# Performance work log

Hardware: AMD Instinct MI355X
Metric: run time of the kernel (lower is better)

Reference implementation:

```python
import jax, jax.numpy as jnp
import numpy as np

N = 50000      # nodes
F_IN = 128     # node_features
T = 12         # periods
E = 800000     # edges (avg degree 16)
MID = 32       # mid_channels (fixed in __init__)
NEG_SLOPE = 0.01
EPS = 1e-12


def setup_inputs() -> dict:
    key = jax.random.key(0)
    ks = jax.random.split(key, 9)
    s_in = 1.0 / np.sqrt(F_IN)
    s_mid = 1.0 / np.sqrt(MID)
    return {
        "x": jax.random.normal(ks[0], (1, N, F_IN, T), jnp.float32),
        "edge_index": jax.random.randint(ks[1], (2, E), 0, N, jnp.int64),
        "edge_weight": jax.random.uniform(ks[2], (E,), jnp.float32),
        # SAGEConv params: lin_l (with bias) applied to aggregated neighbors, lin_r (no bias) to root
        "W_l": jax.random.uniform(ks[3], (MID, F_IN), jnp.float32, -s_in, s_in),
        "b_l": jax.random.uniform(ks[4], (MID,), jnp.float32, -s_in, s_in),
        "W_r": jax.random.uniform(ks[5], (MID, F_IN), jnp.float32, -s_in, s_in),
        "attention": jax.random.uniform(ks[6], (T,), jnp.float32),
        "lin_W": jax.random.uniform(ks[7], (1, MID), jnp.float32, -s_mid, s_mid),
        "lin_b": jax.random.uniform(ks[8], (1,), jnp.float32, -s_mid, s_mid),
    }


def reference(x, edge_index, edge_weight, W_l, b_l, W_r, attention, lin_W, lin_b):
    src, dst = edge_index[0], edge_index[1]
    # in-degree for mean aggregation (shared across periods)
    deg = jax.ops.segment_sum(jnp.ones((E,), x.dtype), dst, num_segments=N)
    inv_deg = 1.0 / jnp.clip(deg, 1.0)  # [N]

    def sage(xt):  # xt: [N, F_IN] -> [N, MID], SAGEConv(mean, normalize=True)
        agg = jax.ops.segment_sum(xt[src], dst, num_segments=N) * inv_deg[:, None]
        out = agg @ W_l.T + b_l + xt @ W_r.T
        norm = jnp.linalg.norm(out, axis=-1, keepdims=True)
        return out / jnp.maximum(norm, EPS)

    gk = jax.random.key(42)
    k1, k2 = jax.random.split(gk)
    # F.gumbel_softmax over the periods-attention vector (tau=1, soft)
    probs = jax.nn.softmax(attention + jax.random.gumbel(k1, (T,), x.dtype))

    h = jnp.zeros((N, MID), x.dtype)
    for t in range(T):  # small fixed unroll over periods
        h = h + probs[t] * sage(x[0, :, :, t])

    h = jnp.where(h > 0, h, NEG_SLOPE * h)        # leaky_relu
    h = h @ lin_W.T + lin_b                        # [N, 1]
    g2 = jax.random.gumbel(k2, h.shape, h.dtype)
    return jax.nn.softmax(h + g2, axis=0)          # gumbel_softmax over nodes
```

## Files before the change

### kernel.cpp

```cpp
#include <hip/hip_runtime.h>
#include <hip/hip_fp16.h>
#include <stdint.h>

#define N_NODES 50000
#define F_INF   128
#define T_P     12
#define N_EDGES 800000
#define MIDC    32
#define SCHUNK  782

typedef __attribute__((ext_vector_type(8))) short bf16x8;
typedef __attribute__((ext_vector_type(4))) float f32x4;

__device__ __forceinline__ uint32_t rotl32(uint32_t v, int r) {
  return (v << r) | (v >> (32 - r));
}

__device__ __forceinline__ void threefry(uint32_t k0, uint32_t k1,
                                         uint32_t x0, uint32_t x1,
                                         uint32_t& o0, uint32_t& o1) {
  uint32_t k2 = k0 ^ k1 ^ 0x1BD11BDAu;
  x0 += k0; x1 += k1;
#define TFR(r) { x0 += x1; x1 = rotl32(x1, r); x1 ^= x0; }
  TFR(13) TFR(15) TFR(26) TFR(6)
  x0 += k1; x1 += k2 + 1u;
  TFR(17) TFR(29) TFR(16) TFR(24)
  x0 += k2; x1 += k0 + 2u;
  TFR(13) TFR(15) TFR(26) TFR(6)
  x0 += k0; x1 += k1 + 3u;
  TFR(17) TFR(29) TFR(16) TFR(24)
  x0 += k1; x1 += k2 + 4u;
  TFR(13) TFR(15) TFR(26) TFR(6)
  x0 += k2; x1 += k0 + 5u;
#undef TFR
  o0 = x0; o1 = x1;
}

__device__ __forceinline__ float gumbel_from_bits(uint32_t bits) {
  const float TINY = 1.17549435082228751e-38f;
  float f = __uint_as_float((bits >> 9) | 0x3F800000u) - 1.0f;
  float u = fmaxf(TINY, f * (1.0f - TINY) + TINY);
  return -logf(-logf(u));
}

__device__ __forceinline__ uint32_t f2bf(float f) {
  uint32_t u = __float_as_uint(f);
  return (u + 0x7FFFu + ((u >> 16) & 1u)) >> 16;
}
__device__ __forceinline__ float bf2f(uint16_t v) {
  return __uint_as_float(((uint32_t)v) << 16);
}

__device__ __forceinline__ uint32_t f2e5m2(float v) {
  float ax = fabsf(v);
  uint32_t s = (__float_as_uint(v) >> 31) << 7;
  if (ax < 6.103515625e-5f) return s;
  ax = fminf(ax, 57344.0f);
  uint32_t u = __float_as_uint(ax);
  u += 0xFFFFFu + ((u >> 21) & 1u);
  uint32_t m = (u >> 21) & 3u;
  uint32_t E = (u >> 23) - 127u + 15u;
  return s | (E << 2) | m;
}

union HU { uint32_t u; __half2 h; };
__device__ __forceinline__ void acc_e5m2(uint32_t u, __half2& lo, __half2& hi) {
  HU a, b;
  a.u = (u << 8) & 0xff00ff00u;
  b.u = u & 0xff00ff00u;
  lo = __hadd2(lo, a.h);
  hi = __hadd2(hi, b.h);
}

__global__ void k_init(const float* __restrict__ att, const float* __restrict__ Wl,
                       const float* __restrict__ Wr,
                       float* __restrict__ header, uint16_t* __restrict__ wtb,
                       int* __restrict__ cnt, int* __restrict__ cursor,
                       float* __restrict__ psum) {
  int bid = blockIdx.x;
  if (bid == 0) {
    if (threadIdx.x == 0) {
      uint32_t a0, a1, b0, b1;
      threefry(0u, 42u, 0u, 0u, a0, a1);
      threefry(0u, 42u, 0u, 1u, b0, b1);
      float v[12], m = -3.4e38f;
      for (int t = 0; t < 12; ++t) {
        uint32_t o0, o1;
        threefry(a0, a1, 0u, (uint32_t)t, o0, o1);
        v[t] = att[t] + gumbel_from_bits(o0 ^ o1);
        m = fmaxf(m, v[t]);
      }
      float s = 0.f;
      for (int t = 0; t < 12; ++t) { v[t] = expf(v[t] - m); s += v[t]; }
      for (int t = 0; t < 12; ++t) header[t] = v[t] / s;
      uint32_t* hu = (uint32_t*)header;
      hu[16] = b0; hu[17] = b1;
    }
  } else if (bid <= 32) {
    int i = (bid - 1) * 256 + threadIdx.x;
    int cm = i >> 7, f = i & 127;
    float val = (cm < 32) ? Wl[cm * 128 + f] : Wr[(cm - 32) * 128 + f];
    wtb[i] = (uint16_t)f2bf(val);
  } else {
    int i = (bid - 33) * 256 + threadIdx.x;
    if (i < N_NODES) cnt[i] = 0;
    else if (i < 2 * N_NODES) cursor[i - N_NODES] = 0;
    else if (i < 2 * N_NODES + 64) psum[i - 2 * N_NODES] = 0.f;
  }
}

__global__ void k_scan1(const int* __restrict__ cnt, int* __restrict__ bsum) {
  __shared__ int sb[256];
  int b = blockIdx.x, tid = threadIdx.x;
  int start = b * SCHUNK, end = min(start + SCHUNK, N_NODES);
  int s = 0;
  for (int i = start + tid; i < end; i += 256) s += cnt[i];
  sb[tid] = s;
  __syncthreads();
  for (int o = 128; o > 0; o >>= 1) {
    if (tid < o) sb[tid] += sb[tid + o];
    __syncthreads();
  }
  if (tid == 0) bsum[b] = sb[0];
}

__global__ void k_scan2(const int* __restrict__ cnt, const int* __restrict__ bsum,
                        int* __restrict__ rowptr) {
  __shared__ int bs[64];
  __shared__ int sc[256];
  int b = blockIdx.x, tid = threadIdx.x;
  if (tid < 64) bs[tid] = bsum[tid];
  __syncthreads();
  int base = 0;
  for (int k = 0; k < b; ++k) base += bs[k];
  int bstart = b * SCHUNK, bend = min(bstart + SCHUNK, N_NODES);
  int istart = bstart + tid * 4;
  int iend = min(istart + 4, bend);
  int c[4]; int s = 0;
#pragma unroll
  for (int k = 0; k < 4; ++k) {
    int i = istart + k;
    c[k] = (i < bend) ? cnt[i] : 0;
    s += c[k];
  }
  sc[tid] = s;
  __syncthreads();
  for (int off = 1; off < 256; off <<= 1) {
    int v = (tid >= off) ? sc[tid - off] : 0;
    __syncthreads();
    sc[tid] += v;
    __syncthreads();
  }
  int run = base + sc[tid] - s;
#pragma unroll
  for (int k = 0; k < 4; ++k) {
    int i = istart + k;
    if (i < bend) { rowptr[i] = run; run += c[k]; }
  }
  if (iend == N_NODES) rowptr[N_NODES] = run;
}

__global__ void k_scatter(const int* __restrict__ src, const int* __restrict__ dst,
                          const int* __restrict__ rowptr, int* __restrict__ cursor,
                          int* __restrict__ col) {
  int e = blockIdx.x * blockDim.x + threadIdx.x;
  if (e < N_EDGES) {
    int d = dst[e];
    int pos = rowptr[d] + atomicAdd(&cursor[d], 1);
    col[pos] = src[e];
  }
}

__launch_bounds__(256)
__global__ void k_project(const float* __restrict__ x, const uint16_t* __restrict__ wtb,
                          const float* __restrict__ bl,
                          uint8_t* __restrict__ Y, uint16_t* __restrict__ OUTI,
                          const int* __restrict__ dst, int* __restrict__ cnt) {
  __shared__ uint32_t smem4[16384];
  char* sm = (char*)smem4;
  int tid = threadIdx.x;
  int node_base = blockIdx.x * 16;

  atomicAdd(&cnt[dst[blockIdx.x * 256 + tid]], 1);

  const uint32_t* wtb32 = (const uint32_t*)wtb;
#pragma unroll
  for (int i0 = 0; i0 < 16; ++i0) {
    int i = i0 * 256 + tid;
    uint32_t v = wtb32[i];
    int cm = i >> 6, c = i & 63;
    *(uint32_t*)(sm + 49152 + cm * 256 + ((c * 4) ^ ((cm & 7) << 4))) = v;
  }

#pragma unroll 4
  for (int i = 0; i < 12; ++i) {
    int p = i * 256 + tid;
    int node = p / 192;
    int rem  = p - node * 192;
    int fpair = rem / 3;
    int tg = rem - fpair * 3;
    const float* xb = x + (uint32_t)(node_base + node) * 1536u + fpair * 24 + tg * 4;
    float4 q0 = *(const float4*)xb;
    float4 q1 = *(const float4*)(xb + 12);
    int mb = node * 12 + tg * 4;
    const float* q0f = (const float*)&q0;
    const float* q1f = (const float*)&q1;
#pragma unroll
    for (int j = 0; j < 4; ++j) {
      int m = mb + j;
      uint32_t wv = f2bf(q0f[j]) | (f2bf(q1f[j]) << 16);
      *(uint32_t*)(sm + m * 256 + ((fpair * 4) ^ ((m & 7) << 4))) = wv;
    }
  }
  __syncthreads();

  int w = tid >> 6, l = tid & 63;
  int li = l & 15, kg = l >> 4;
  f32x4 acc[3][4];
#pragma unroll
  for (int mt = 0; mt < 3; ++mt)
#pragma unroll
    for (int nt = 0; nt < 4; ++nt)
      acc[mt][nt] = (f32x4){0.f, 0.f, 0.f, 0.f};

  const char* A = sm;
  const char* B = sm + 49152;
  __builtin_amdgcn_s_setprio(1);
#pragma unroll
  for (int ks = 0; ks < 4; ++ks) {
    int kb = ks * 64 + kg * 16;
    bf16x8 bf0, bf1, bf2, bf3;
    {
      int r0 = li,      s0 = kb ^ ((r0 & 7) << 4);
      int r1 = 16 + li, s1 = kb ^ ((r1 & 7) << 4);
      int r2 = 32 + li, s2 = kb ^ ((r2 & 7) << 4);
      int r3 = 48 + li, s3 = kb ^ ((r3 & 7) << 4);
      bf0 = *(const bf16x8*)(B + r0 * 256 + s0);
      bf1 = *(const bf16x8*)(B + r1 * 256 + s1);
      bf2 = *(const bf16x8*)(B + r2 * 256 + s2);
      bf3 = *(const bf16x8*)(B + r3 * 256 + s3);
    }
#pragma unroll
    for (int mt = 0; mt < 3; ++mt) {
      int row = w * 48 + mt * 16 + li;
      bf16x8 af = *(const bf16x8*)(A + row * 256 + (kb ^ ((row & 7) << 4)));
      acc[mt][0] = __builtin_amdgcn_mfma_f32_16x16x32_bf16(af, bf0, acc[mt][0], 0, 0, 0);
      acc[mt][1] = __builtin_amdgcn_mfma_f32_16x16x32_bf16(af, bf1, acc[mt][1], 0, 0, 0);
      acc[mt][2] = __builtin_amdgcn_mfma_f32_16x16x32_bf16(af, bf2, acc[mt][2], 0, 0, 0);
      acc[mt][3] = __builtin_amdgcn_mfma_f32_16x16x32_bf16(af, bf3, acc[mt][3], 0, 0, 0);
    }
  }
  __builtin_amdgcn_s_setprio(0);

  float bv0 = bl[li], bv1 = bl[16 + li];
#pragma unroll
  for (int mt = 0; mt < 3; ++mt) {
    int rbase = w * 48 + mt * 16 + kg * 4;
#pragma unroll
    for (int r = 0; r < 4; ++r) {
      int m = rbase + r;
      int node = m / 12;
      int t = m - node * 12;
      uint32_t rowoff = (uint32_t)(node_base + node) * 384u + t * 32;
      Y[rowoff + li]      = (uint8_t)f2e5m2(acc[mt][0][r]);
      Y[rowoff + 16 + li] = (uint8_t)f2e5m2(acc[mt][1][r]);
      OUTI[rowoff + li]      = (uint16_t)f2bf(acc[mt][2][r] + bv0);
      OUTI[rowoff + 16 + li] = (uint16_t)f2bf(acc[mt][3][r] + bv1);
    }
  }
}

__launch_bounds__(384)
__global__ void k_gather(const uint8_t* __restrict__ Y, const uint16_t* __restrict__ OUTI,
                         const int* __restrict__ rowptr, const int* __restrict__ col,
                         const float* __restrict__ header,
                         const float* __restrict__ linW, const float* __restrict__ linb,
                         float* __restrict__ out, float* __restrict__ psum) {
  __shared__ float hb[4][12][33];
  __shared__ float esum;
  int tid = threadIdx.x;
  int ln = tid / 96;
  int tc = tid - ln * 96;
  int n = blockIdx.x * 4 + ln;
  int t = tc >> 3, cq = tc & 7;
  if (tid == 0) esum = 0.f;

  int beg = rowptr[n], end = rowptr[n + 1];
  const uint32_t* Yp = reinterpret_cast<const uint32_t*>(Y);
  uint32_t utc = (uint32_t)tc;
  __half2 zl; { HU z; z.u = 0; zl = z.h; }
  __half2 alo = zl, ahi = zl, blo = zl, bhi = zl;
  int j = beg;
  for (; j < end && (j & 3); ++j)
    acc_e5m2(Yp[(uint32_t)col[j] * 96u + utc], alo, ahi);
  for (; j + 7 < end; j += 8) {
    int4 c0 = *reinterpret_cast<const int4*>(&col[j]);
    int4 c1 = *reinterpret_cast<const int4*>(&col[j + 4]);
    uint32_t u0 = Yp[(uint32_t)c0.x * 96u + utc];
    uint32_t u1 = Yp[(uint32_t)c0.y * 96u + utc];
    uint32_t u2 = Yp[(uint32_t)c0.z * 96u + utc];
    uint32_t u3 = Yp[(uint32_t)c0.w * 96u + utc];
    uint32_t u4 = Yp[(uint32_t)c1.x * 96u + utc];
    uint32_t u5 = Yp[(uint32_t)c1.y * 96u + utc];
    uint32_t u6 = Yp[(uint32_t)c1.z * 96u + utc];
    uint32_t u7 = Yp[(uint32_t)c1.w * 96u + utc];
    acc_e5m2(u0, alo, ahi); acc_e5m2(u1, blo, bhi);
    acc_e5m2(u2, alo, ahi); acc_e5m2(u3, blo, bhi);
    acc_e5m2(u4, alo, ahi); acc_e5m2(u5, blo, bhi);
    acc_e5m2(u6, alo, ahi); acc_e5m2(u7, blo, bhi);
  }
  for (; j + 3 < end; j += 4) {
    int4 c0 = *reinterpret_cast<const int4*>(&col[j]);
    uint32_t u0 = Yp[(uint32_t)c0.x * 96u + utc];
    uint32_t u1 = Yp[(uint32_t)c0.y * 96u + utc];
    uint32_t u2 = Yp[(uint32_t)c0.z * 96u + utc];
    uint32_t u3 = Yp[(uint32_t)c0.w * 96u + utc];
    acc_e5m2(u0, alo, ahi); acc_e5m2(u1, blo, bhi);
    acc_e5m2(u2, alo, ahi); acc_e5m2(u3, blo, bhi);
  }
  for (; j < end; ++j)
    acc_e5m2(Yp[(uint32_t)col[j] * 96u + utc], alo, ahi);
  alo = __hadd2(alo, blo); ahi = __hadd2(ahi, bhi);
  float a0 = __low2float(alo),  a2 = __high2float(alo);
  float a1 = __low2float(ahi),  a3 = __high2float(ahi);

  float invd = 1.0f / fmaxf((float)(end - beg), 1.0f);
  ushort4 ov = *reinterpret_cast<const ushort4*>(OUTI + (uint32_t)n * 384u + tc * 4);
  float v0 = bf2f(ov.x) + a0 * invd;
  float v1 = bf2f(ov.y) + a1 * invd;
  float v2 = bf2f(ov.z) + a2 * invd;
  float v3 = bf2f(ov.w) + a3 * invd;
  float sq = v0 * v0 + v1 * v1 + v2 * v2 + v3 * v3;
  sq += __shfl_xor(sq, 1);
  sq += __shfl_xor(sq, 2);
  sq += __shfl_xor(sq, 4);
  float rn = header[t] / fmaxf(sqrtf(sq), 1e-12f);
  float* hrow = &hb[ln][t][cq * 4];
  hrow[0] = v0 * rn; hrow[1] = v1 * rn; hrow[2] = v2 * rn; hrow[3] = v3 * rn;
  __syncthreads();
  if (tid < 128) {
    int ln2 = tid >> 5, c = tid & 31;
    float h = 0.f;
#pragma unroll
    for (int tt = 0; tt < 12; ++tt) h += hb[ln2][tt][c];
    h = (h > 0.f) ? h : 0.01f * h;
    float hv = h * linW[c];
#pragma unroll
    for (int m = 16; m >= 1; m >>= 1) hv += __shfl_xor(hv, m);
    if (c == 0) {
      int n2 = blockIdx.x * 4 + ln2;
      const uint32_t* hu = (const uint32_t*)header;
      uint32_t o0, o1;
      threefry(hu[16], hu[17], 0u, (uint32_t)n2, o0, o1);
      float ex = expf(hv + linb[0] + gumbel_from_bits(o0 ^ o1));
      out[n2] = ex;
      atomicAdd(&esum, ex);
    }
  }
  __syncthreads();
  if (tid == 0) atomicAdd(&psum[blockIdx.x & 63], esum);
}

__global__ void k_scale(float* __restrict__ out, const float* __restrict__ psum) {
  float S = 0.f;
#pragma unroll
  for (int k = 0; k < 64; ++k) S += psum[k];
  int i = blockIdx.x * blockDim.x + threadIdx.x;
  if (i < N_NODES) out[i] = out[i] / S;
}

extern "C" void kernel_launch(void* const* d_in, const int* in_sizes, int n_in,
                              void* d_out, int out_size, void* d_ws, size_t ws_size,
                              hipStream_t stream) {
  (void)in_sizes; (void)n_in; (void)out_size; (void)ws_size;
  const float* x    = (const float*)d_in[0];
  const int*   ei   = (const int*)d_in[1];
  const float* Wl   = (const float*)d_in[3];
  const float* bl   = (const float*)d_in[4];
  const float* Wr   = (const float*)d_in[5];
  const float* att  = (const float*)d_in[6];
  const float* linW = (const float*)d_in[7];
  const float* linb = (const float*)d_in[8];
  float* out = (float*)d_out;

  const int* esrc = ei;
  const int* edst = ei + N_EDGES;

  char* base = (char*)d_ws;
  size_t o = 0;
  auto take = [&](size_t b) { size_t r = o; o += (b + 255) & ~(size_t)255; return r; };
  float* header = (float*)(base + take(256));
  int*   cnt    = (int*)(base + take((size_t)N_NODES * 4));
  int*   cursor = (int*)(base + take((size_t)N_NODES * 4));
  int*   rowptr = (int*)(base + take((size_t)(N_NODES + 1) * 4));
  int*   col    = (int*)(base + take((size_t)N_EDGES * 4));
  int*   bsum   = (int*)(base + take(64 * 4));
  float* psum   = (float*)(base + take(64 * 4));
  uint16_t* wtb = (uint16_t*)(base + take(64 * 128 * 2));
  uint8_t*  Y   = (uint8_t*)(base + take((size_t)N_NODES * 384));
  uint16_t* OUTI= (uint16_t*)(base + take((size_t)N_NODES * 384 * 2));

  k_init<<<424, 256, 0, stream>>>(att, Wl, Wr, header, wtb, cnt, cursor, psum);
  k_project<<<N_NODES / 16, 256, 0, stream>>>(x, wtb, bl, Y, OUTI, edst, cnt);
  k_scan1<<<64, 256, 0, stream>>>(cnt, bsum);
  k_scan2<<<64, 256, 0, stream>>>(cnt, bsum, rowptr);
  k_scatter<<<(N_EDGES + 255) / 256, 256, 0, stream>>>(esrc, edst, rowptr, cursor, col);
  k_gather<<<N_NODES / 4, 384, 0, stream>>>(Y, OUTI, rowptr, col, header, linW, linb, out, psum);
  k_scale<<<(N_NODES + 255) / 256, 256, 0, stream>>>(out, psum);
}
```

Baseline: 241.7 us.

## Quantize projected neighbor features to FP4 e2m1 and widen gather per thread

Projected neighbor features, which the gather step reads randomly, are now stored as 4-bit e2m1 values instead of 8-bit e5m2. This halves the Y buffer and the bytes fetched per edge. The gather kernel decodes them with a byte-permute lookup into half2 accumulators and now handles 8 nodes per block, with each thread covering 8 channels. The projection epilogue uses a transposed MFMA operand order so that stores can be packed. The cursor reset moves from init into scan2. FP4 quantization of aggregated features is very coarse and risks accuracy failures against the reference.

```diff
diff --git a/kernel.cpp b/kernel.cpp
--- a/kernel.cpp
+++ b/kernel.cpp
@@ -51,32 +51,37 @@
   return __uint_as_float(((uint32_t)v) << 16);
 }
 
-__device__ __forceinline__ uint32_t f2e5m2(float v) {
+__device__ __forceinline__ uint32_t f2e2m1(float v) {
   float ax = fabsf(v);
-  uint32_t s = (__float_as_uint(v) >> 31) << 7;
-  if (ax < 6.103515625e-5f) return s;
-  ax = fminf(ax, 57344.0f);
-  uint32_t u = __float_as_uint(ax);
-  u += 0xFFFFFu + ((u >> 21) & 1u);
-  uint32_t m = (u >> 21) & 3u;
-  uint32_t E = (u >> 23) - 127u + 15u;
-  return s | (E << 2) | m;
+  uint32_t s = (__float_as_uint(v) >> 31) << 3;
+  if (ax < 0.75f) return s | (ax <= 0.25f ? 0u : 1u);
+  uint32_t u = __float_as_uint(fminf(fmaxf(ax, 1.0f), 6.0f));
+  u += 0x1FFFFFu + ((u >> 22) & 1u);
+  uint32_t m = (u >> 22) & 1u;
+  uint32_t E = (u >> 23) - 127u;
+  return s | (((E + 1u) << 1) | m);
 }
 
 union HU { uint32_t u; __half2 h; };
-__device__ __forceinline__ void acc_e5m2(uint32_t u, __half2& lo, __half2& hi) {
+__device__ __forceinline__ void acc_fp4(uint32_t u, __half2& e0, __half2& e1,
+                                        __half2& o0, __half2& o1) {
+  uint32_t ue = u & 0x0F0F0F0Fu;
+  uint32_t uo = (u >> 4) & 0x0F0F0F0Fu;
+  uint32_t pe = __builtin_amdgcn_perm(0x46444240u, 0x3E3C3800u, ue & 0x07070707u)
+              | ((ue & 0x08080808u) << 4);
+  uint32_t po = __builtin_amdgcn_perm(0x46444240u, 0x3E3C3800u, uo & 0x07070707u)
+              | ((uo & 0x08080808u) << 4);
   HU a, b;
-  a.u = (u << 8) & 0xff00ff00u;
-  b.u = u & 0xff00ff00u;
-  lo = __hadd2(lo, a.h);
-  hi = __hadd2(hi, b.h);
+  a.u = (pe << 8) & 0xff00ff00u; e0 = __hadd2(e0, a.h);
+  b.u = pe & 0xff00ff00u;        e1 = __hadd2(e1, b.h);
+  a.u = (po << 8) & 0xff00ff00u; o0 = __hadd2(o0, a.h);
+  b.u = po & 0xff00ff00u;        o1 = __hadd2(o1, b.h);
 }
 
 __global__ void k_init(const float* __restrict__ att, const float* __restrict__ Wl,
                        const float* __restrict__ Wr,
                        float* __restrict__ header, uint16_t* __restrict__ wtb,
-                       int* __restrict__ cnt, int* __restrict__ cursor,
-                       float* __restrict__ psum) {
+                       int* __restrict__ cnt, float* __restrict__ psum) {
   int bid = blockIdx.x;
   if (bid == 0) {
     if (threadIdx.x == 0) {
@@ -104,8 +109,7 @@
   } else {
     int i = (bid - 33) * 256 + threadIdx.x;
     if (i < N_NODES) cnt[i] = 0;
-    else if (i < 2 * N_NODES) cursor[i - N_NODES] = 0;
-    else if (i < 2 * N_NODES + 64) psum[i - 2 * N_NODES] = 0.f;
+    else if (i < N_NODES + 64) psum[i - N_NODES] = 0.f;
   }
 }
 
@@ -125,7 +129,7 @@
 }
 
 __global__ void k_scan2(const int* __restrict__ cnt, const int* __restrict__ bsum,
-                        int* __restrict__ rowptr) {
+                        int* __restrict__ rowptr, int* __restrict__ cursor) {
   __shared__ int bs[64];
   __shared__ int sc[256];
   int b = blockIdx.x, tid = threadIdx.x;
@@ -155,7 +159,7 @@
 #pragma unroll
   for (int k = 0; k < 4; ++k) {
     int i = istart + k;
-    if (i < bend) { rowptr[i] = run; run += c[k]; }
+    if (i < bend) { rowptr[i] = run; cursor[i] = 0; run += c[k]; }
   }
   if (iend == N_NODES) rowptr[N_NODES] = run;
 }
@@ -218,10 +222,10 @@
   int li = l & 15, kg = l >> 4;
   f32x4 acc[3][4];
 #pragma unroll
-  for (int mt = 0; mt < 3; ++mt)
-#pragma unroll
-    for (int nt = 0; nt < 4; ++nt)
-      acc[mt][nt] = (f32x4){0.f, 0.f, 0.f, 0.f};
+  for (int jt = 0; jt < 3; ++jt)
+#pragma unroll
+    for (int it = 0; it < 4; ++it)
+      acc[jt][it] = (f32x4){0.f, 0.f, 0.f, 0.f};
 
   const char* A = sm;
   const char* B = sm + 49152;
@@ -229,44 +233,52 @@
 #pragma unroll
   for (int ks = 0; ks < 4; ++ks) {
     int kb = ks * 64 + kg * 16;
-    bf16x8 bf0, bf1, bf2, bf3;
+    bf16x8 wf0, wf1, wf2, wf3;
     {
       int r0 = li,      s0 = kb ^ ((r0 & 7) << 4);
       int r1 = 16 + li, s1 = kb ^ ((r1 & 7) << 4);
       int r2 = 32 + li, s2 = kb ^ ((r2 & 7) << 4);
       int r3 = 48 + li, s3 = kb ^ ((r3 & 7) << 4);
-      bf0 = *(const bf16x8*)(B + r0 * 256 + s0);
-      bf1 = *(const bf16x8*)(B + r1 * 256 + s1);
-      bf2 = *(const bf16x8*)(B + r2 * 256 + s2);
-      bf3 = *(const bf16x8*)(B + r3 * 256 + s3);
-    }
-#pragma unroll
-    for (int mt = 0; mt < 3; ++mt) {
-      int row = w * 48 + mt * 16 + li;
-      bf16x8 af = *(const bf16x8*)(A + row * 256 + (kb ^ ((row & 7) << 4)));
-      acc[mt][0] = __builtin_amdgcn_mfma_f32_16x16x32_bf16(af, bf0, acc[mt][0], 0, 0, 0);
-      acc[mt][1] = __builtin_amdgcn_mfma_f32_16x16x32_bf16(af, bf1, acc[mt][1], 0, 0, 0);
-      acc[mt][2] = __builtin_amdgcn_mfma_f32_16x16x32_bf16(af, bf2, acc[mt][2], 0, 0, 0);
-      acc[mt][3] = __builtin_amdgcn_mfma_f32_16x16x32_bf16(af, bf3, acc[mt][3], 0, 0, 0);
+      wf0 = *(const bf16x8*)(B + r0 * 256 + s0);
+      wf1 = *(const bf16x8*)(B + r1 * 256 + s1);
+      wf2 = *(const bf16x8*)(B + r2 * 256 + s2);
+      wf3 = *(const bf16x8*)(B + r3 * 256 + s3);
+    }
+#pragma unroll
+    for (int jt = 0; jt < 3; ++jt) {
+      int row = w * 48 + jt * 16 + li;
+      bf16x8 xf = *(const bf16x8*)(A + row * 256 + (kb ^ ((row & 7) << 4)));
+      acc[jt][0] = __builtin_amdgcn_mfma_f32_16x16x32_bf16(wf0, xf, acc[jt][0], 0, 0, 0);
+      acc[jt][1] = __builtin_amdgcn_mfma_f32_16x16x32_bf16(wf1, xf, acc[jt][1], 0, 0, 0);
+      acc[jt][2] = __builtin_amdgcn_mfma_f32_16x16x32_bf16(wf2, xf, acc[jt][2], 0, 0, 0);
+      acc[jt][3] = __builtin_amdgcn_mfma_f32_16x16x32_bf16(wf3, xf, acc[jt][3], 0, 0, 0);
     }
   }
   __builtin_amdgcn_s_setprio(0);
 
-  float bv0 = bl[li], bv1 = bl[16 + li];
-#pragma unroll
-  for (int mt = 0; mt < 3; ++mt) {
-    int rbase = w * 48 + mt * 16 + kg * 4;
-#pragma unroll
-    for (int r = 0; r < 4; ++r) {
-      int m = rbase + r;
-      int node = m / 12;
-      int t = m - node * 12;
-      uint32_t rowoff = (uint32_t)(node_base + node) * 384u + t * 32;
-      Y[rowoff + li]      = (uint8_t)f2e5m2(acc[mt][0][r]);
-      Y[rowoff + 16 + li] = (uint8_t)f2e5m2(acc[mt][1][r]);
-      OUTI[rowoff + li]      = (uint16_t)f2bf(acc[mt][2][r] + bv0);
-      OUTI[rowoff + 16 + li] = (uint16_t)f2bf(acc[mt][3][r] + bv1);
-    }
+  float4 bla = *(const float4*)&bl[kg * 4];
+  float4 blb = *(const float4*)&bl[16 + kg * 4];
+#pragma unroll
+  for (int jt = 0; jt < 3; ++jt) {
+    int m = (w * 3 + jt) * 16 + li;
+    int node = m / 12;
+    int t = m - node * 12;
+    uint32_t rbY = (uint32_t)(node_base + node) * 192u + t * 16;
+#pragma unroll
+    for (int it = 0; it < 2; ++it) {
+      uint32_t p = 0;
+#pragma unroll
+      for (int r = 0; r < 4; ++r) p |= f2e2m1(acc[jt][it][r]) << (4 * r);
+      *(uint16_t*)(Y + rbY + it * 8 + kg * 2) = (uint16_t)p;
+    }
+    uint32_t rbO = (uint32_t)(node_base + node) * 384u + t * 32;
+    uint2 pk;
+    pk.x = f2bf(acc[jt][2][0] + bla.x) | (f2bf(acc[jt][2][1] + bla.y) << 16);
+    pk.y = f2bf(acc[jt][2][2] + bla.z) | (f2bf(acc[jt][2][3] + bla.w) << 16);
+    *(uint2*)(OUTI + rbO + kg * 4) = pk;
+    pk.x = f2bf(acc[jt][3][0] + blb.x) | (f2bf(acc[jt][3][1] + blb.y) << 16);
+    pk.y = f2bf(acc[jt][3][2] + blb.z) | (f2bf(acc[jt][3][3] + blb.w) << 16);
+    *(uint2*)(OUTI + rbO + 16 + kg * 4) = pk;
   }
 }
 
@@ -276,69 +288,77 @@
                          const float* __restrict__ header,
                          const float* __restrict__ linW, const float* __restrict__ linb,
                          float* __restrict__ out, float* __restrict__ psum) {
-  __shared__ float hb[4][12][33];
+  __shared__ float hb[8][12][33];
   __shared__ float esum;
   int tid = threadIdx.x;
-  int ln = tid / 96;
-  int tc = tid - ln * 96;
-  int n = blockIdx.x * 4 + ln;
-  int t = tc >> 3, cq = tc & 7;
+  int ln = tid / 48;
+  int tc = tid - ln * 48;
+  int n = blockIdx.x * 8 + ln;
+  int t = tc >> 2, cq = tc & 3;
   if (tid == 0) esum = 0.f;
 
   int beg = rowptr[n], end = rowptr[n + 1];
   const uint32_t* Yp = reinterpret_cast<const uint32_t*>(Y);
   uint32_t utc = (uint32_t)tc;
   __half2 zl; { HU z; z.u = 0; zl = z.h; }
-  __half2 alo = zl, ahi = zl, blo = zl, bhi = zl;
+  __half2 ae0 = zl, ae1 = zl, ao0 = zl, ao1 = zl;
+  __half2 be0 = zl, be1 = zl, bo0 = zl, bo1 = zl;
   int j = beg;
   for (; j < end && (j & 3); ++j)
-    acc_e5m2(Yp[(uint32_t)col[j] * 96u + utc], alo, ahi);
+    acc_fp4(Yp[(uint32_t)col[j] * 48u + utc], ae0, ae1, ao0, ao1);
   for (; j + 7 < end; j += 8) {
     int4 c0 = *reinterpret_cast<const int4*>(&col[j]);
     int4 c1 = *reinterpret_cast<const int4*>(&col[j + 4]);
-    uint32_t u0 = Yp[(uint32_t)c0.x * 96u + utc];
-    uint32_t u1 = Yp[(uint32_t)c0.y * 96u + utc];
-    uint32_t u2 = Yp[(uint32_t)c0.z * 96u + utc];
-    uint32_t u3 = Yp[(uint32_t)c0.w * 96u + utc];
-    uint32_t u4 = Yp[(uint32_t)c1.x * 96u + utc];
-    uint32_t u5 = Yp[(uint32_t)c1.y * 96u + utc];
-    uint32_t u6 = Yp[(uint32_t)c1.z * 96u + utc];
-    uint32_t u7 = Yp[(uint32_t)c1.w * 96u + utc];
-    acc_e5m2(u0, alo, ahi); acc_e5m2(u1, blo, bhi);
-    acc_e5m2(u2, alo, ahi); acc_e5m2(u3, blo, bhi);
-    acc_e5m2(u4, alo, ahi); acc_e5m2(u5, blo, bhi);
-    acc_e5m2(u6, alo, ahi); acc_e5m2(u7, blo, bhi);
+    uint32_t u0 = Yp[(uint32_t)c0.x * 48u + utc];
+    uint32_t u1 = Yp[(uint32_t)c0.y * 48u + utc];
+    uint32_t u2 = Yp[(uint32_t)c0.z * 48u + utc];
+    uint32_t u3 = Yp[(uint32_t)c0.w * 48u + utc];
+    uint32_t u4 = Yp[(uint32_t)c1.x * 48u + utc];
+    uint32_t u5 = Yp[(uint32_t)c1.y * 48u + utc];
+    uint32_t u6 = Yp[(uint32_t)c1.z * 48u + utc];
+    uint32_t u7 = Yp[(uint32_t)c1.w * 48u + utc];
+    acc_fp4(u0, ae0, ae1, ao0, ao1); acc_fp4(u1, be0, be1, bo0, bo1);
+    acc_fp4(u2, ae0, ae1, ao0, ao1); acc_fp4(u3, be0, be1, bo0, bo1);
+    acc_fp4(u4, ae0, ae1, ao0, ao1); acc_fp4(u5, be0, be1, bo0, bo1);
+    acc_fp4(u6, ae0, ae1, ao0, ao1); acc_fp4(u7, be0, be1, bo0, bo1);
   }
   for (; j + 3 < end; j += 4) {
     int4 c0 = *reinterpret_cast<const int4*>(&col[j]);
-    uint32_t u0 = Yp[(uint32_t)c0.x * 96u + utc];
-    uint32_t u1 = Yp[(uint32_t)c0.y * 96u + utc];
-    uint32_t u2 = Yp[(uint32_t)c0.z * 96u + utc];
-    uint32_t u3 = Yp[(uint32_t)c0.w * 96u + utc];
-    acc_e5m2(u0, alo, ahi); acc_e5m2(u1, blo, bhi);
-    acc_e5m2(u2, alo, ahi); acc_e5m2(u3, blo, bhi);
+    uint32_t u0 = Yp[(uint32_t)c0.x * 48u + utc];
+    uint32_t u1 = Yp[(uint32_t)c0.y * 48u + utc];
+    uint32_t u2 = Yp[(uint32_t)c0.z * 48u + utc];
+    uint32_t u3 = Yp[(uint32_t)c0.w * 48u + utc];
+    acc_fp4(u0, ae0, ae1, ao0, ao1); acc_fp4(u1, be0, be1, bo0, bo1);
+    acc_fp4(u2, ae0, ae1, ao0, ao1); acc_fp4(u3, be0, be1, bo0, bo1);
   }
   for (; j < end; ++j)
-    acc_e5m2(Yp[(uint32_t)col[j] * 96u + utc], alo, ahi);
-  alo = __hadd2(alo, blo); ahi = __hadd2(ahi, bhi);
-  float a0 = __low2float(alo),  a2 = __high2float(alo);
-  float a1 = __low2float(ahi),  a3 = __high2float(ahi);
+    acc_fp4(Yp[(uint32_t)col[j] * 48u + utc], ae0, ae1, ao0, ao1);
+  ae0 = __hadd2(ae0, be0); ae1 = __hadd2(ae1, be1);
+  ao0 = __hadd2(ao0, bo0); ao1 = __hadd2(ao1, bo1);
+  float a0 = __low2float(ae0), a4 = __high2float(ae0);
+  float a2 = __low2float(ae1), a6 = __high2float(ae1);
+  float a1 = __low2float(ao0), a5 = __high2float(ao0);
+  float a3 = __low2float(ao1), a7 = __high2float(ao1);
 
   float invd = 1.0f / fmaxf((float)(end - beg), 1.0f);
-  ushort4 ov = *reinterpret_cast<const ushort4*>(OUTI + (uint32_t)n * 384u + tc * 4);
-  float v0 = bf2f(ov.x) + a0 * invd;
-  float v1 = bf2f(ov.y) + a1 * invd;
-  float v2 = bf2f(ov.z) + a2 * invd;
-  float v3 = bf2f(ov.w) + a3 * invd;
-  float sq = v0 * v0 + v1 * v1 + v2 * v2 + v3 * v3;
+  uint4 ov = *reinterpret_cast<const uint4*>(OUTI + (uint32_t)n * 384u + tc * 8);
+  float v0 = bf2f((uint16_t)(ov.x & 0xffff)) + a0 * invd;
+  float v1 = bf2f((uint16_t)(ov.x >> 16))    + a1 * invd;
+  float v2 = bf2f((uint16_t)(ov.y & 0xffff)) + a2 * invd;
+  float v3 = bf2f((uint16_t)(ov.y >> 16))    + a3 * invd;
+  float v4 = bf2f((uint16_t)(ov.z & 0xffff)) + a4 * invd;
+  float v5 = bf2f((uint16_t)(ov.z >> 16))    + a5 * invd;
+  float v6 = bf2f((uint16_t)(ov.w & 0xffff)) + a6 * invd;
+  float v7 = bf2f((uint16_t)(ov.w >> 16))    + a7 * invd;
+  float sq = v0*v0 + v1*v1 + v2*v2 + v3*v3 + v4*v4 + v5*v5 + v6*v6 + v7*v7;
   sq += __shfl_xor(sq, 1);
   sq += __shfl_xor(sq, 2);
-  sq += __shfl_xor(sq, 4);
   float rn = header[t] / fmaxf(sqrtf(sq), 1e-12f);
-  float* hrow = &hb[ln][t][cq * 4];
+  float* hrow = &hb[ln][t][cq * 8];
   hrow[0] = v0 * rn; hrow[1] = v1 * rn; hrow[2] = v2 * rn; hrow[3] = v3 * rn;
-  __syncthreads();
-  if (tid < 128) {
+  hrow[4] = v4 * rn; hrow[5] = v5 * rn; hrow[6] = v6 * rn; hrow[7] = v7 * rn;
+  __syncthreads();
+  if (tid < 256) {
     int ln2 = tid >> 5, c = tid & 31;
     float h = 0.f;
 #pragma unroll
@@ -348,7 +368,7 @@
 #pragma unroll
     for (int m = 16; m >= 1; m >>= 1) hv += __shfl_xor(hv, m);
     if (c == 0) {
-      int n2 = blockIdx.x * 4 + ln2;
+      int n2 = blockIdx.x * 8 + ln2;
       const uint32_t* hu = (const uint32_t*)header;
       uint32_t o0, o1;
       threefry(hu[16], hu[17], 0u, (uint32_t)n2, o0, o1);
@@ -397,14 +417,14 @@
   int*   bsum   = (int*)(base + take(64 * 4));
   float* psum   = (float*)(base + take(64 * 4));
   uint16_t* wtb = (uint16_t*)(base + take(64 * 128 * 2));
-  uint8_t*  Y   = (uint8_t*)(base + take((size_t)N_NODES * 384));
+  uint8_t*  Y   = (uint8_t*)(base + take((size_t)N_NODES * 192));
   uint16_t* OUTI= (uint16_t*)(base + take((size_t)N_NODES * 384 * 2));
 
-  k_init<<<424, 256, 0, stream>>>(att, Wl, Wr, header, wtb, cnt, cursor, psum);
+  k_init<<<230, 256, 0, stream>>>(att, Wl, Wr, header, wtb, cnt, psum);
   k_project<<<N_NODES / 16, 256, 0, stream>>>(x, wtb, bl, Y, OUTI, edst, cnt);
   k_scan1<<<64, 256, 0, stream>>>(cnt, bsum);
-  k_scan2<<<64, 256, 0, stream>>>(cnt, bsum, rowptr);
+  k_scan2<<<64, 256, 0, stream>>>(cnt, bsum, rowptr, cursor);
   k_scatter<<<(N_EDGES + 255) / 256, 256, 0, stream>>>(esrc, edst, rowptr, cursor, col);
-  k_gather<<<N_NODES / 4, 384, 0, stream>>>(Y, OUTI, rowptr, col, header, linW, linb, out, psum);
+  k_gather<<<N_NODES / 8, 384, 0, stream>>>(Y, OUTI, rowptr, col, header, linW, linb, out, psum);
   k_scale<<<(N_NODES + 255) / 256, 256, 0, stream>>>(out, psum);
 }
```

New measurement: 207.7 us. 1.16x faster.
